# Kernel tuning notes

Measured on AMD Instinct MI355X. Metric: run time of the kernel, lower is better.

The kernel has to match this reference:

```python
import jax, jax.numpy as jnp
import numpy as np

EPS = 1e-6
THRESHOLD = 0.99
MAX_STEPS = 4
MIN_STEPS = 1
N_HEAD = 8
B, N, D, V, L, F, RCF = 1, 256, 512, 32000, 2, 1536, 2048


def rmsnorm(x, w):
    return x * jax.lax.rsqrt(jnp.mean(x * x, axis=-1, keepdims=True) + EPS) * w


def rope(x, base=10000.0):
    # x: [B, N, H, hd] -> rotary embedding (rotate-half convention)
    n, hd = x.shape[1], x.shape[-1]
    half = hd // 2
    inv = 1.0 / (base ** (jnp.arange(half, dtype=jnp.float32) * 2.0 / hd))
    ang = jnp.arange(n, dtype=jnp.float32)[:, None] * inv[None, :]  # [N, half]
    cos = jnp.cos(ang)[None, :, None, :]
    sin = jnp.sin(ang)[None, :, None, :]
    x1, x2 = x[..., :half], x[..., half:]
    return jnp.concatenate([x1 * cos - x2 * sin, x1 * sin + x2 * cos], axis=-1)


def attention(x, wqkv, wo):
    b, n, d = x.shape
    hd = d // N_HEAD
    q, k, v = jnp.split(x @ wqkv, 3, axis=-1)
    q = rope(q.reshape(b, n, N_HEAD, hd))
    k = rope(k.reshape(b, n, N_HEAD, hd))
    v = v.reshape(b, n, N_HEAD, hd)
    scores = jnp.einsum('bqhd,bkhd->bhqk', q, k) / np.float32(np.sqrt(hd))
    causal = jnp.tril(jnp.ones((n, n), dtype=bool))
    scores = jnp.where(causal, scores, jnp.float32(-1e30))
    a = jax.nn.softmax(scores, axis=-1)
    out = jnp.einsum('bhqk,bkhd->bqhd', a, v).reshape(b, n, d)
    return out @ wo


def backbone(input_ids, emb, attn_norm_w, mlp_norm_w, wqkv, wo, w_gate, w_up, w_down, final_norm_w):
    x = emb[input_ids]  # [B, N, D]
    for l in range(L):  # small fixed layer count
        x = x + attention(rmsnorm(x, attn_norm_w[l]), wqkv[l], wo[l])
        h = rmsnorm(x, mlp_norm_w[l])
        x = x + (jax.nn.silu(h @ w_gate[l]) * (h @ w_up[l])) @ w_down[l]  # SwiGLU
    return rmsnorm(x, final_norm_w)


def refinement_step(states, rc_norm_w, rc_w1, rc_w2, w_y, w_delta, w_halt, b_halt):
    h = rmsnorm(states, rc_norm_w)
    y_logits = h @ w_y                                   # [B, N, V]
    refined = states + jax.nn.gelu(h @ rc_w1) @ rc_w2    # [B, N, D]
    delta_logits = rmsnorm(refined, rc_norm_w) @ w_delta # [B, N, V]
    halt = jax.nn.sigmoid(h @ w_halt + b_halt)           # [B, N]
    combined = y_logits + delta_logits                   # compute_prediction
    return combined, halt, refined


def act_combine(halt_probs, step_logits):
    # Vectorized version of the per-(b,n) ACT halting loop.
    # halt_probs: [B, N, S]; step_logits: [B, N, S, V]
    p = halt_probs.at[..., :MIN_STEPS].set(0.0)  # min-step masking (max_steps > min_steps)
    cum = jnp.cumsum(p, axis=-1)
    prev = cum - p                      # exclusive cumulative halting prob
    running = prev < THRESHOLD          # step still executes
    is_last = jnp.arange(p.shape[-1]) == p.shape[-1] - 1
    use_rem = running & ((cum >= THRESHOLD) | is_last)  # halting step gets remainder
    weights = jnp.where(running, jnp.where(use_rem, 1.0 - prev, p), 0.0)
    final = jnp.einsum('bns,bnsv->bnv', weights, step_logits)
    remainder = jnp.sum(jnp.where(use_rem, 1.0 - prev, 0.0), axis=-1)
    ponder = jnp.sum(running, axis=-1).astype(p.dtype) + remainder  # N + R ponder cost
    return final, ponder, weights


def reference(input_ids, emb, attn_norm_w, mlp_norm_w, wqkv, wo, w_gate, w_up, w_down,
              final_norm_w, rc_norm_w, rc_w1, rc_w2, w_y, w_delta, w_halt, b_halt):
    hidden = backbone(input_ids, emb, attn_norm_w, mlp_norm_w, wqkv, wo,
                      w_gate, w_up, w_down, final_norm_w)
    states = hidden
    logits_steps, halt_steps = [], []
    for _ in range(MAX_STEPS):  # fixed refinement unroll
        combined, halt, states = refinement_step(states, rc_norm_w, rc_w1, rc_w2,
                                                 w_y, w_delta, w_halt, b_halt)
        logits_steps.append(combined)
        halt_steps.append(halt)
    step_logits = jnp.stack(logits_steps, axis=2)  # [B, N, S, V]
    halt_probs = jnp.stack(halt_steps, axis=2)     # [B, N, S]
    final_logits, ponder_costs, all_weights = act_combine(halt_probs, step_logits)
    return final_logits, ponder_costs, all_weights


def setup_inputs() -> dict:
    key = jax.random.key(0)
    ks = jax.random.split(key, 16)
    s = 0.02
    return {
        'input_ids': jax.random.randint(ks[0], (B, N), 0, V),
        'emb': jax.random.normal(ks[1], (V, D), jnp.float32) * s,
        'attn_norm_w': jnp.ones((L, D), jnp.float32),
        'mlp_norm_w': jnp.ones((L, D), jnp.float32),
        'wqkv': jax.random.normal(ks[2], (L, D, 3 * D), jnp.float32) * s,
        'wo': jax.random.normal(ks[3], (L, D, D), jnp.float32) * s,
        'w_gate': jax.random.normal(ks[4], (L, D, F), jnp.float32) * s,
        'w_up': jax.random.normal(ks[5], (L, D, F), jnp.float32) * s,
        'w_down': jax.random.normal(ks[6], (L, F, D), jnp.float32) * s,
        'final_norm_w': jnp.ones((D,), jnp.float32),
        'rc_norm_w': jnp.ones((D,), jnp.float32),
        'rc_w1': jax.random.normal(ks[7], (D, RCF), jnp.float32) * s,
        'rc_w2': jax.random.normal(ks[8], (RCF, D), jnp.float32) * s,
        'w_y': jax.random.normal(ks[9], (D, V), jnp.float32) * s,
        'w_delta': jax.random.normal(ks[10], (D, V), jnp.float32) * s,
        'w_halt': jax.random.normal(ks[11], (D,), jnp.float32) * s,
        'b_halt': jnp.zeros((), jnp.float32),
    }
```

## Files before the change

### kernel.cpp

```cpp
#include <hip/hip_runtime.h>
#include <hip/hip_bf16.h>

#define NTOK   256
#define DMODEL 512
#define NHEAD  8
#define HD     64
#define HALF   32
#define FF     1536
#define RCFF   2048
#define VOCAB  32000
#define NLAYER 2
#define NSTEPS 4
#define EPSV   1e-6f
#define THR    0.99f

typedef __attribute__((ext_vector_type(8))) short bf16x8;
typedef __attribute__((ext_vector_type(4))) float f32x4;

__global__ void k_embed(const int* __restrict__ ids, const float* __restrict__ emb,
                        float* __restrict__ x) {
    int row = blockIdx.x;
    int id = ids[row];
    for (int d = threadIdx.x; d < DMODEL; d += blockDim.x)
        x[row * DMODEL + d] = emb[(size_t)id * DMODEL + d];
}

__global__ __launch_bounds__(256) void k_rmsnorm(const float* __restrict__ in,
                                                 const float* __restrict__ w,
                                                 float* __restrict__ out) {
    int row = blockIdx.x;
    const float* xr = in + (size_t)row * DMODEL;
    float s = 0.f;
    for (int d = threadIdx.x; d < DMODEL; d += 256) { float v = xr[d]; s += v * v; }
    __shared__ float red[4];
    int lane = threadIdx.x & 63, wv = threadIdx.x >> 6;
    for (int o = 32; o > 0; o >>= 1) s += __shfl_xor(s, o);
    if (lane == 0) red[wv] = s;
    __syncthreads();
    float tot = red[0] + red[1] + red[2] + red[3];
    float scale = rsqrtf(tot * (1.f / DMODEL) + EPSV);
    for (int d = threadIdx.x; d < DMODEL; d += 256)
        out[(size_t)row * DMODEL + d] = xr[d] * scale * w[d];
}

__global__ __launch_bounds__(256) void k_mm_part(const float* __restrict__ A,
                                                 const float* __restrict__ W,
                                                 float* __restrict__ Cp,
                                                 int K, int N, int kc) {
    __shared__ float As[16][68];
    __shared__ float Ws[16][68];
    const int bn = blockIdx.x * 64;
    const int bm = blockIdx.y * 64;
    const int kz = blockIdx.z * kc;
    const int tx = threadIdx.x & 15;
    const int ty = threadIdx.x >> 4;
    float acc[4][4] = {};
    for (int k0 = kz; k0 < kz + kc; k0 += 16) {
#pragma unroll
        for (int r = 0; r < 4; ++r) {
            int idx = threadIdx.x + r * 256;
            int m = idx >> 4, kk = idx & 15;
            As[kk][m] = A[(size_t)(bm + m) * K + k0 + kk];
            int n = idx & 63, kw = idx >> 6;
            Ws[kw][n] = W[(size_t)(k0 + kw) * N + bn + n];
        }
        __syncthreads();
#pragma unroll
        for (int kk = 0; kk < 16; ++kk) {
            float4 av = *(const float4*)&As[kk][ty * 4];
            float4 bv = *(const float4*)&Ws[kk][tx * 4];
            float a[4] = {av.x, av.y, av.z, av.w};
            float b[4] = {bv.x, bv.y, bv.z, bv.w};
#pragma unroll
            for (int i = 0; i < 4; ++i)
#pragma unroll
                for (int j = 0; j < 4; ++j)
                    acc[i][j] = fmaf(a[i], b[j], acc[i][j]);
        }
        __syncthreads();
    }
    float* cp = Cp + (size_t)blockIdx.z * (size_t)(gridDim.y * 64) * N;
#pragma unroll
    for (int i = 0; i < 4; ++i) {
        int m = bm + ty * 4 + i;
#pragma unroll
        for (int j = 0; j < 4; ++j)
            cp[(size_t)m * N + bn + tx * 4 + j] = acc[i][j];
    }
}

__global__ __launch_bounds__(256) void k_gu_part(const float* __restrict__ A,
                                                 const float* __restrict__ Wg,
                                                 const float* __restrict__ Wu,
                                                 float* __restrict__ GU) {
    __shared__ float As[16][68];
    __shared__ float Ws[16][68];
    const int bn = blockIdx.x * 64;
    const int bm = blockIdx.y * 64;
    const int z = blockIdx.z;
    const float* W = (z >> 2) ? Wu : Wg;
    const int kz = (z & 3) * 128;
    const int tx = threadIdx.x & 15;
    const int ty = threadIdx.x >> 4;
    float acc[4][4] = {};
    for (int k0 = kz; k0 < kz + 128; k0 += 16) {
#pragma unroll
        for (int r = 0; r < 4; ++r) {
            int idx = threadIdx.x + r * 256;
            int m = idx >> 4, kk = idx & 15;
            As[kk][m] = A[(size_t)(bm + m) * DMODEL + k0 + kk];
            int n = idx & 63, kw = idx >> 6;
            Ws[kw][n] = W[(size_t)(k0 + kw) * FF + bn + n];
        }
        __syncthreads();
#pragma unroll
        for (int kk = 0; kk < 16; ++kk) {
            float4 av = *(const float4*)&As[kk][ty * 4];
            float4 bv = *(const float4*)&Ws[kk][tx * 4];
            float a[4] = {av.x, av.y, av.z, av.w};
            float b[4] = {bv.x, bv.y, bv.z, bv.w};
#pragma unroll
            for (int i = 0; i < 4; ++i)
#pragma unroll
                for (int j = 0; j < 4; ++j)
                    acc[i][j] = fmaf(a[i], b[j], acc[i][j]);
        }
        __syncthreads();
    }
    float* cp = GU + (size_t)z * (NTOK * FF);
#pragma unroll
    for (int i = 0; i < 4; ++i) {
        int m = bm + ty * 4 + i;
#pragma unroll
        for (int j = 0; j < 4; ++j)
            cp[(size_t)m * FF + bn + tx * 4 + j] = acc[i][j];
    }
}

__global__ void k_mm_finish(const float* __restrict__ Cp, const float* __restrict__ res,
                            float* __restrict__ C, int tot, int zstride, int nz, int act) {
    int i = blockIdx.x * 256 + threadIdx.x;
    if (i >= tot) return;
    float s = 0.f;
    for (int z = 0; z < nz; ++z) s += Cp[(size_t)z * zstride + i];
    if (res) s += res[i];
    if (act == 1) {
        float xg = s;
        float inner = 0.79788456080286536f * (xg + 0.044715f * xg * xg * xg);
        s = 0.5f * xg * (1.f + tanhf(inner));
    }
    C[i] = s;
}

__global__ void k_finish_silumul(const float* __restrict__ GU, float* __restrict__ C) {
    int i = blockIdx.x * 256 + threadIdx.x;
    float g = 0.f, u = 0.f;
#pragma unroll
    for (int z = 0; z < 4; ++z) {
        g += GU[(size_t)z * (NTOK * FF) + i];
        u += GU[(size_t)(z + 4) * (NTOK * FF) + i];
    }
    float sig = 1.f / (1.f + expf(-g));
    C[i] = g * sig * u;
}

__global__ __launch_bounds__(256) void k_finish_norm(const float* __restrict__ Cp,
                                                     const float* __restrict__ res,
                                                     const float* __restrict__ normw,
                                                     float* __restrict__ out_raw,
                                                     float* __restrict__ out_norm,
                                                     int nz) {
    int row = blockIdx.x, t = threadIdx.x;
    int c0 = t, c1 = t + 256;
    size_t base = (size_t)row * DMODEL;
    float v0 = 0.f, v1 = 0.f;
    for (int z = 0; z < nz; ++z) {
        size_t zb = (size_t)z * (NTOK * DMODEL) + base;
        v0 += Cp[zb + c0];
        v1 += Cp[zb + c1];
    }
    v0 += res[base + c0];
    v1 += res[base + c1];
    float ss = v0 * v0 + v1 * v1;
    __shared__ float red[4];
    int lane = t & 63, wv = t >> 6;
    for (int o = 32; o > 0; o >>= 1) ss += __shfl_xor(ss, o);
    if (lane == 0) red[wv] = ss;
    __syncthreads();
    float tot = red[0] + red[1] + red[2] + red[3];
    float scale = rsqrtf(tot * (1.f / DMODEL) + EPSV);
    out_raw[base + c0] = v0;
    out_raw[base + c1] = v1;
    out_norm[base + c0] = v0 * scale * normw[c0];
    out_norm[base + c1] = v1 * scale * normw[c1];
}

__global__ __launch_bounds__(256) void k_qkv_finish_rope(const float* __restrict__ Cp,
                                                         float* __restrict__ qkv) {
    int pos = blockIdx.x, t = threadIdx.x;
    int h = t >> 5, d = t & 31;
    size_t base = (size_t)pos * FF;
    auto S = [&](int col) {
        float s = 0.f;
#pragma unroll
        for (int z = 0; z < 4; ++z) s += Cp[(size_t)z * (NTOK * FF) + base + col];
        return s;
    };
    int cq0 = h * HD + d, cq1 = cq0 + HALF;
    int ck0 = DMODEL + cq0, ck1 = ck0 + HALF;
    int cv0 = 2 * DMODEL + t, cv1 = cv0 + 256;
    float q0 = S(cq0), q1 = S(cq1);
    float k0 = S(ck0), k1 = S(ck1);
    float v0 = S(cv0), v1 = S(cv1);
    float inv = powf(10000.f, -(float)d / 32.f);
    float ang = (float)pos * inv;
    float c = cosf(ang), s = sinf(ang);
    qkv[base + cq0] = q0 * c - q1 * s;
    qkv[base + cq1] = q0 * s + q1 * c;
    qkv[base + ck0] = k0 * c - k1 * s;
    qkv[base + ck1] = k0 * s + k1 * c;
    qkv[base + cv0] = v0;
    qkv[base + cv1] = v1;
}

__global__ __launch_bounds__(256) void k_attn(const float* __restrict__ qkv,
                                              float* __restrict__ out) {
    int h = blockIdx.x;
    int qi = blockIdx.y;
    int t = threadIdx.x;
    __shared__ float qs[HD];
    __shared__ float ps[NTOK];
    __shared__ float red[4];
    __shared__ float red2[4];
    __shared__ float os[4][HD];
    if (t < HD) qs[t] = qkv[(size_t)qi * FF + h * HD + t];
    __syncthreads();
    float sc = -1e30f;
    if (t <= qi) {
        const float* kr = qkv + (size_t)t * FF + DMODEL + h * HD;
        float s = 0.f;
        for (int d = 0; d < HD; ++d) s = fmaf(qs[d], kr[d], s);
        sc = s * 0.125f;
    }
    float m = sc;
    for (int o = 32; o > 0; o >>= 1) m = fmaxf(m, __shfl_xor(m, o));
    int lane = t & 63, wv = t >> 6;
    if (lane == 0) red[wv] = m;
    __syncthreads();
    m = fmaxf(fmaxf(red[0], red[1]), fmaxf(red[2], red[3]));
    float e = (t <= qi) ? expf(sc - m) : 0.f;
    ps[t] = e;
    float sum = e;
    for (int o = 32; o > 0; o >>= 1) sum += __shfl_xor(sum, o);
    if (lane == 0) red2[wv] = sum;
    __syncthreads();
    sum = red2[0] + red2[1] + red2[2] + red2[3];
    float inv = 1.f / sum;
    int d = t & 63, g = t >> 6;
    float acc = 0.f;
    for (int ki = g; ki <= qi; ki += 4)
        acc = fmaf(ps[ki], qkv[(size_t)ki * FF + 2 * DMODEL + h * HD + d], acc);
    os[g][d] = acc * inv;
    __syncthreads();
    if (t < HD)
        out[(size_t)qi * DMODEL + h * HD + t] = os[0][t] + os[1][t] + os[2][t] + os[3][t];
}

__global__ __launch_bounds__(256) void k_haltactab(const float* __restrict__ H,
                                                   const float* __restrict__ wh,
                                                   const float* __restrict__ bptr,
                                                   float* __restrict__ ponder_out,
                                                   float* __restrict__ w_out,
                                                   __hip_bfloat16* __restrict__ A,
                                                   __hip_bfloat16* __restrict__ Bm) {
    int i = blockIdx.x, t = threadIdx.x;
    int lane = t & 63, wv = t >> 6;
    __shared__ float red[4];
    __shared__ float hvals[3];
    __shared__ float hw[4];
    for (int s = 1; s <= 3; ++s) {
        const float* hr = H + ((size_t)s * NTOK + i) * DMODEL;
        float a = hr[t] * wh[t] + hr[t + 256] * wh[t + 256];
        for (int o = 32; o > 0; o >>= 1) a += __shfl_xor(a, o);
        if (lane == 0) red[wv] = a;
        __syncthreads();
        if (t == 0)
            hvals[s - 1] = 1.f / (1.f + expf(-(red[0] + red[1] + red[2] + red[3] + bptr[0])));
        __syncthreads();
    }
    if (t == 0) {
        float p[4] = {0.f, hvals[0], hvals[1], hvals[2]};
        float cum = 0.f, rem = 0.f;
        int nrun = 0;
#pragma unroll
        for (int s = 0; s < 4; ++s) {
            float prev = cum;
            cum += p[s];
            bool running = prev < THR;
            bool use_rem = running && ((cum >= THR) || (s == 3));
            float v = 0.f;
            if (running) {
                v = use_rem ? (1.f - prev) : p[s];
                if (use_rem) rem += (1.f - prev);
                nrun++;
            }
            hw[s] = v;
            w_out[i * 4 + s] = v;
        }
        ponder_out[i] = (float)nrun + rem;
    }
    __syncthreads();
    float w0 = hw[0], w1 = hw[1], w2 = hw[2], w3 = hw[3];
    size_t base = (size_t)i * DMODEL;
#pragma unroll
    for (int r = 0; r < 2; ++r) {
        int d = t + r * 256;
        float h0 = H[base + d];
        float h1 = H[(size_t)(NTOK * DMODEL) + base + d];
        float h2 = H[(size_t)(2 * NTOK * DMODEL) + base + d];
        float h3 = H[(size_t)(3 * NTOK * DMODEL) + base + d];
        float h4 = H[(size_t)(4 * NTOK * DMODEL) + base + d];
        A[base + d]  = __float2bfloat16(w0 * h0 + w1 * h1 + w2 * h2 + w3 * h3);
        Bm[base + d] = __float2bfloat16(w0 * h1 + w1 * h2 + w2 * h3 + w3 * h4);
    }
}

__global__ __launch_bounds__(512) void k_logits_mfma(const __hip_bfloat16* __restrict__ Abf,
                                                     const __hip_bfloat16* __restrict__ Bbf,
                                                     const float* __restrict__ Wy,
                                                     const float* __restrict__ Wd,
                                                     float* __restrict__ out) {
    __shared__ short Alds[256 * 32];
    __shared__ short Blds[256 * 32];
    __shared__ short Wys[32 * 70];
    __shared__ short Wds[32 * 70];
    const int tid  = threadIdx.x;
    const int wave = tid >> 6;
    const int lane = tid & 63;
    const int wrow = (wave & 1) * 128;
    const int wcol = (wave >> 1) * 16;
    const int cl   = lane & 15;
    const int kg   = lane >> 4;
    const int col  = blockIdx.x * 64 + wcol + cl;

    const int kr = tid >> 4;
    const int c4 = (tid & 15) * 4;
    const int sr0 = tid >> 2;
    const int skp = (tid & 3) * 8;

    f32x4 acc[8];
#pragma unroll
    for (int i = 0; i < 8; ++i) acc[i] = (f32x4){0.f, 0.f, 0.f, 0.f};

    const float* gy = Wy + (size_t)kr * VOCAB + blockIdx.x * 64 + c4;
    const float* gd = Wd + (size_t)kr * VOCAB + blockIdx.x * 64 + c4;

    float4 ry = *(const float4*)gy;
    float4 rd = *(const float4*)gd;
    bf16x8 ra0 = *(const bf16x8*)(Abf + (size_t)sr0 * DMODEL + skp);
    bf16x8 ra1 = *(const bf16x8*)(Abf + (size_t)(sr0 + 128) * DMODEL + skp);
    bf16x8 rb0 = *(const bf16x8*)(Bbf + (size_t)sr0 * DMODEL + skp);
    bf16x8 rb1 = *(const bf16x8*)(Bbf + (size_t)(sr0 + 128) * DMODEL + skp);

    for (int t = 0; t < 16; ++t) {
        __syncthreads();
        {
            short2 a, b;
            a.x = (short)__hip_bfloat16_raw(__float2bfloat16(ry.x)).x;
            a.y = (short)__hip_bfloat16_raw(__float2bfloat16(ry.y)).x;
            b.x = (short)__hip_bfloat16_raw(__float2bfloat16(ry.z)).x;
            b.y = (short)__hip_bfloat16_raw(__float2bfloat16(ry.w)).x;
            *(short2*)&Wys[kr * 70 + c4]     = a;
            *(short2*)&Wys[kr * 70 + c4 + 2] = b;
            a.x = (short)__hip_bfloat16_raw(__float2bfloat16(rd.x)).x;
            a.y = (short)__hip_bfloat16_raw(__float2bfloat16(rd.y)).x;
            b.x = (short)__hip_bfloat16_raw(__float2bfloat16(rd.z)).x;
            b.y = (short)__hip_bfloat16_raw(__float2bfloat16(rd.w)).x;
            *(short2*)&Wds[kr * 70 + c4]     = a;
            *(short2*)&Wds[kr * 70 + c4 + 2] = b;
            *(bf16x8*)&Alds[sr0 * 32 + skp]         = ra0;
            *(bf16x8*)&Alds[(sr0 + 128) * 32 + skp] = ra1;
            *(bf16x8*)&Blds[sr0 * 32 + skp]         = rb0;
            *(bf16x8*)&Blds[(sr0 + 128) * 32 + skp] = rb1;
        }
        if (t < 15) {
            const int kn = (t + 1) * 32;
            ry  = *(const float4*)(gy + (size_t)(t + 1) * 32 * VOCAB);
            rd  = *(const float4*)(gd + (size_t)(t + 1) * 32 * VOCAB);
            ra0 = *(const bf16x8*)(Abf + (size_t)sr0 * DMODEL + kn + skp);
            ra1 = *(const bf16x8*)(Abf + (size_t)(sr0 + 128) * DMODEL + kn + skp);
            rb0 = *(const bf16x8*)(Bbf + (size_t)sr0 * DMODEL + kn + skp);
            rb1 = *(const bf16x8*)(Bbf + (size_t)(sr0 + 128) * DMODEL + kn + skp);
        }
        __syncthreads();
        bf16x8 wy, wd;
#pragma unroll
        for (int j = 0; j < 8; ++j) {
            wy[j] = Wys[(kg * 8 + j) * 70 + wcol + cl];
            wd[j] = Wds[(kg * 8 + j) * 70 + wcol + cl];
        }
#pragma unroll
        for (int mt = 0; mt < 8; ++mt) {
            const int row = wrow + mt * 16 + cl;
            const bf16x8 a = *(const bf16x8*)&Alds[row * 32 + kg * 8];
            const bf16x8 b = *(const bf16x8*)&Blds[row * 32 + kg * 8];
            acc[mt] = __builtin_amdgcn_mfma_f32_16x16x32_bf16(a, wy, acc[mt], 0, 0, 0);
            acc[mt] = __builtin_amdgcn_mfma_f32_16x16x32_bf16(b, wd, acc[mt], 0, 0, 0);
        }
    }
#pragma unroll
    for (int mt = 0; mt < 8; ++mt)
#pragma unroll
        for (int r = 0; r < 4; ++r)
            out[(size_t)(wrow + mt * 16 + kg * 4 + r) * VOCAB + col] = acc[mt][r];
}

extern "C" void kernel_launch(void* const* d_in, const int* in_sizes, int n_in,
                              void* d_out, int out_size, void* d_ws, size_t ws_size,
                              hipStream_t stream) {
    const int*   ids          = (const int*)d_in[0];
    const float* emb          = (const float*)d_in[1];
    const float* attn_norm_w  = (const float*)d_in[2];
    const float* mlp_norm_w   = (const float*)d_in[3];
    const float* wqkv         = (const float*)d_in[4];
    const float* wo           = (const float*)d_in[5];
    const float* w_gate       = (const float*)d_in[6];
    const float* w_up         = (const float*)d_in[7];
    const float* w_down       = (const float*)d_in[8];
    const float* final_norm_w = (const float*)d_in[9];
    const float* rc_norm_w    = (const float*)d_in[10];
    const float* rc_w1        = (const float*)d_in[11];
    const float* rc_w2        = (const float*)d_in[12];
    const float* w_y          = (const float*)d_in[13];
    const float* w_delta      = (const float*)d_in[14];
    const float* w_halt       = (const float*)d_in[15];
    const float* b_halt       = (const float*)d_in[16];
    float* out = (float*)d_out;

    float* ws = (float*)d_ws;
    float* x       = ws + 0;
    float* xn      = ws + 131072;
    float* qkv     = ws + 262144;
    float* attnout = ws + 655360;
    float* g       = ws + 786432;
    float* t1      = ws + 1179648;
    float* states  = ws + 1703936;
    float* states2 = ws + 1835008;
    float* H       = ws + 1966080;
    __hip_bfloat16* Abf = (__hip_bfloat16*)(ws + 2623488);
    __hip_bfloat16* Bbf = (__hip_bfloat16*)(ws + 2754560);
    float* Cp      = ws + 2885632;
    float* GU      = ws + 1179648;

    k_embed<<<NTOK, 256, 0, stream>>>(ids, emb, x);
    k_rmsnorm<<<NTOK, 256, 0, stream>>>(x, attn_norm_w, xn);
    for (int l = 0; l < NLAYER; ++l) {
        k_mm_part<<<dim3(FF / 64, 4, 4), 256, 0, stream>>>(
            xn, wqkv + (size_t)l * DMODEL * FF, Cp, DMODEL, FF, 128);
        k_qkv_finish_rope<<<NTOK, 256, 0, stream>>>(Cp, qkv);
        k_attn<<<dim3(NHEAD, NTOK), 256, 0, stream>>>(qkv, attnout);
        k_mm_part<<<dim3(DMODEL / 64, 4, 8), 256, 0, stream>>>(
            attnout, wo + (size_t)l * DMODEL * DMODEL, Cp, DMODEL, DMODEL, 64);
        k_finish_norm<<<NTOK, 256, 0, stream>>>(Cp, x, mlp_norm_w + l * DMODEL, x, xn, 8);
        k_gu_part<<<dim3(FF / 64, 4, 8), 256, 0, stream>>>(
            xn, w_gate + (size_t)l * DMODEL * FF, w_up + (size_t)l * DMODEL * FF, GU);
        k_finish_silumul<<<NTOK * FF / 256, 256, 0, stream>>>(GU, g);
        k_mm_part<<<dim3(DMODEL / 64, 4, 12), 256, 0, stream>>>(
            g, w_down + (size_t)l * FF * DMODEL, Cp, FF, DMODEL, 128);
        const float* nw = (l == 0) ? (attn_norm_w + DMODEL) : final_norm_w;
        float* nout = (l == 0) ? xn : states;
        k_finish_norm<<<NTOK, 256, 0, stream>>>(Cp, x, nw, x, nout, 12);
    }

    k_rmsnorm<<<NTOK, 256, 0, stream>>>(states, rc_norm_w, H);
    float* scur = states;
    float* snxt = states2;
    for (int s = 0; s < NSTEPS; ++s) {
        k_mm_part<<<dim3(RCFF / 64, 4, 4), 256, 0, stream>>>(
            H + (size_t)s * NTOK * DMODEL, rc_w1, Cp, DMODEL, RCFF, 128);
        k_mm_finish<<<NTOK * RCFF / 256, 256, 0, stream>>>(
            Cp, nullptr, t1, NTOK * RCFF, NTOK * RCFF, 4, 1);
        k_mm_part<<<dim3(DMODEL / 64, 4, 16), 256, 0, stream>>>(
            t1, rc_w2, Cp, RCFF, DMODEL, 128);
        k_finish_norm<<<NTOK, 256, 0, stream>>>(
            Cp, scur, rc_norm_w, snxt, H + (size_t)(s + 1) * NTOK * DMODEL, 16);
        float* tmp = scur; scur = snxt; snxt = tmp;
    }

    k_haltactab<<<NTOK, 256, 0, stream>>>(H, w_halt, b_halt,
                                          out + (size_t)NTOK * VOCAB,
                                          out + (size_t)NTOK * VOCAB + NTOK,
                                          Abf, Bbf);

    k_logits_mfma<<<VOCAB / 64, 512, 0, stream>>>(Abf, Bbf, w_y, w_delta, out);
}
```

Baseline: 382.3 us.

## Enlarge fp32 GEMM M-tile to 128 with float4 loads; split logits over rows

The fp32 SIMT GEMM kernels now compute 128x64 tiles, eight rows per thread, and load A and W with float4 global reads. This is meant to raise arithmetic intensity and cut global load instructions, at the cost of more registers and half as many blocks. The MFMA logits kernel is split into two row halves on a 2D grid, doubling block count for occupancy but loading each W tile twice.

After: 475.2 us. +24.3%, slower.

```diff
diff --git a/kernel.cpp b/kernel.cpp
--- a/kernel.cpp
+++ b/kernel.cpp
@@ -43,84 +43,98 @@
         out[(size_t)row * DMODEL + d] = xr[d] * scale * w[d];
 }
 
-__global__ __launch_bounds__(256) void k_mm_part(const float* __restrict__ A,
-                                                 const float* __restrict__ W,
-                                                 float* __restrict__ Cp,
-                                                 int K, int N, int kc) {
-    __shared__ float As[16][68];
+__global__ __launch_bounds__(256) void k_mm_part2(const float* __restrict__ A,
+                                                  const float* __restrict__ W,
+                                                  float* __restrict__ Cp,
+                                                  int K, int N, int kc) {
+    __shared__ float As[16][132];
     __shared__ float Ws[16][68];
     const int bn = blockIdx.x * 64;
-    const int bm = blockIdx.y * 64;
+    const int bm = blockIdx.y * 128;
     const int kz = blockIdx.z * kc;
     const int tx = threadIdx.x & 15;
     const int ty = threadIdx.x >> 4;
-    float acc[4][4] = {};
+    float acc[8][4] = {};
     for (int k0 = kz; k0 < kz + kc; k0 += 16) {
 #pragma unroll
-        for (int r = 0; r < 4; ++r) {
-            int idx = threadIdx.x + r * 256;
-            int m = idx >> 4, kk = idx & 15;
-            As[kk][m] = A[(size_t)(bm + m) * K + k0 + kk];
-            int n = idx & 63, kw = idx >> 6;
-            Ws[kw][n] = W[(size_t)(k0 + kw) * N + bn + n];
+        for (int r = 0; r < 2; ++r) {
+            int f = threadIdx.x + r * 256;
+            int row = f >> 2, kq = (f & 3) * 4;
+            float4 v = *(const float4*)&A[(size_t)(bm + row) * K + k0 + kq];
+            As[kq + 0][row] = v.x;
+            As[kq + 1][row] = v.y;
+            As[kq + 2][row] = v.z;
+            As[kq + 3][row] = v.w;
+        }
+        {
+            int kw = threadIdx.x >> 4, n4 = (threadIdx.x & 15) * 4;
+            *(float4*)&Ws[kw][n4] = *(const float4*)&W[(size_t)(k0 + kw) * N + bn + n4];
         }
         __syncthreads();
 #pragma unroll
         for (int kk = 0; kk < 16; ++kk) {
-            float4 av = *(const float4*)&As[kk][ty * 4];
+            float4 a0 = *(const float4*)&As[kk][ty * 8];
+            float4 a1 = *(const float4*)&As[kk][ty * 8 + 4];
             float4 bv = *(const float4*)&Ws[kk][tx * 4];
-            float a[4] = {av.x, av.y, av.z, av.w};
+            float a[8] = {a0.x, a0.y, a0.z, a0.w, a1.x, a1.y, a1.z, a1.w};
             float b[4] = {bv.x, bv.y, bv.z, bv.w};
 #pragma unroll
-            for (int i = 0; i < 4; ++i)
+            for (int i = 0; i < 8; ++i)
 #pragma unroll
                 for (int j = 0; j < 4; ++j)
                     acc[i][j] = fmaf(a[i], b[j], acc[i][j]);
         }
         __syncthreads();
     }
-    float* cp = Cp + (size_t)blockIdx.z * (size_t)(gridDim.y * 64) * N;
-#pragma unroll
-    for (int i = 0; i < 4; ++i) {
-        int m = bm + ty * 4 + i;
+    float* cp = Cp + (size_t)blockIdx.z * (size_t)(gridDim.y * 128) * N;
+#pragma unroll
+    for (int i = 0; i < 8; ++i) {
+        int m = bm + ty * 8 + i;
 #pragma unroll
         for (int j = 0; j < 4; ++j)
             cp[(size_t)m * N + bn + tx * 4 + j] = acc[i][j];
     }
 }
 
-__global__ __launch_bounds__(256) void k_gu_part(const float* __restrict__ A,
-                                                 const float* __restrict__ Wg,
-                                                 const float* __restrict__ Wu,
-                                                 float* __restrict__ GU) {
-    __shared__ float As[16][68];
+__global__ __launch_bounds__(256) void k_gu_part2(const float* __restrict__ A,
+                                                  const float* __restrict__ Wg,
+                                                  const float* __restrict__ Wu,
+                                                  float* __restrict__ GU) {
+    __shared__ float As[16][132];
     __shared__ float Ws[16][68];
     const int bn = blockIdx.x * 64;
-    const int bm = blockIdx.y * 64;
+    const int bm = blockIdx.y * 128;
     const int z = blockIdx.z;
     const float* W = (z >> 2) ? Wu : Wg;
     const int kz = (z & 3) * 128;
     const int tx = threadIdx.x & 15;
     const int ty = threadIdx.x >> 4;
-    float acc[4][4] = {};
+    float acc[8][4] = {};
     for (int k0 = kz; k0 < kz + 128; k0 += 16) {
 #pragma unroll
-        for (int r = 0; r < 4; ++r) {
-            int idx = threadIdx.x + r * 256;
-            int m = idx >> 4, kk = idx & 15;
-            As[kk][m] = A[(size_t)(bm + m) * DMODEL + k0 + kk];
-            int n = idx & 63, kw = idx >> 6;
-            Ws[kw][n] = W[(size_t)(k0 + kw) * FF + bn + n];
+        for (int r = 0; r < 2; ++r) {
+            int f = threadIdx.x + r * 256;
+            int row = f >> 2, kq = (f & 3) * 4;
+            float4 v = *(const float4*)&A[(size_t)(bm + row) * DMODEL + k0 + kq];
+            As[kq + 0][row] = v.x;
+            As[kq + 1][row] = v.y;
+            As[kq + 2][row] = v.z;
+            As[kq + 3][row] = v.w;
+        }
+        {
+            int kw = threadIdx.x >> 4, n4 = (threadIdx.x & 15) * 4;
+            *(float4*)&Ws[kw][n4] = *(const float4*)&W[(size_t)(k0 + kw) * FF + bn + n4];
         }
         __syncthreads();
 #pragma unroll
         for (int kk = 0; kk < 16; ++kk) {
-            float4 av = *(const float4*)&As[kk][ty * 4];
+            float4 a0 = *(const float4*)&As[kk][ty * 8];
+            float4 a1 = *(const float4*)&As[kk][ty * 8 + 4];
             float4 bv = *(const float4*)&Ws[kk][tx * 4];
-            float a[4] = {av.x, av.y, av.z, av.w};
+            float a[8] = {a0.x, a0.y, a0.z, a0.w, a1.x, a1.y, a1.z, a1.w};
             float b[4] = {bv.x, bv.y, bv.z, bv.w};
 #pragma unroll
-            for (int i = 0; i < 4; ++i)
+            for (int i = 0; i < 8; ++i)
 #pragma unroll
                 for (int j = 0; j < 4; ++j)
                     acc[i][j] = fmaf(a[i], b[j], acc[i][j]);
@@ -129,8 +143,8 @@
     }
     float* cp = GU + (size_t)z * (NTOK * FF);
 #pragma unroll
-    for (int i = 0; i < 4; ++i) {
-        int m = bm + ty * 4 + i;
+    for (int i = 0; i < 8; ++i) {
+        int m = bm + ty * 8 + i;
 #pragma unroll
         for (int j = 0; j < 4; ++j)
             cp[(size_t)m * FF + bn + tx * 4 + j] = acc[i][j];
@@ -330,14 +344,15 @@
                                                      const float* __restrict__ Wy,
                                                      const float* __restrict__ Wd,
                                                      float* __restrict__ out) {
-    __shared__ short Alds[256 * 32];
-    __shared__ short Blds[256 * 32];
+    __shared__ short Alds[128 * 32];
+    __shared__ short Blds[128 * 32];
     __shared__ short Wys[32 * 70];
     __shared__ short Wds[32 * 70];
     const int tid  = threadIdx.x;
     const int wave = tid >> 6;
     const int lane = tid & 63;
-    const int wrow = (wave & 1) * 128;
+    const int rbase = blockIdx.y * 128;
+    const int wrow = (wave & 1) * 64;
     const int wcol = (wave >> 1) * 16;
     const int cl   = lane & 15;
     const int kg   = lane >> 4;
@@ -345,22 +360,20 @@
 
     const int kr = tid >> 4;
     const int c4 = (tid & 15) * 4;
-    const int sr0 = tid >> 2;
+    const int sr = tid >> 2;
     const int skp = (tid & 3) * 8;
 
-    f32x4 acc[8];
-#pragma unroll
-    for (int i = 0; i < 8; ++i) acc[i] = (f32x4){0.f, 0.f, 0.f, 0.f};
+    f32x4 acc[4];
+#pragma unroll
+    for (int i = 0; i < 4; ++i) acc[i] = (f32x4){0.f, 0.f, 0.f, 0.f};
 
     const float* gy = Wy + (size_t)kr * VOCAB + blockIdx.x * 64 + c4;
     const float* gd = Wd + (size_t)kr * VOCAB + blockIdx.x * 64 + c4;
 
     float4 ry = *(const float4*)gy;
     float4 rd = *(const float4*)gd;
-    bf16x8 ra0 = *(const bf16x8*)(Abf + (size_t)sr0 * DMODEL + skp);
-    bf16x8 ra1 = *(const bf16x8*)(Abf + (size_t)(sr0 + 128) * DMODEL + skp);
-    bf16x8 rb0 = *(const bf16x8*)(Bbf + (size_t)sr0 * DMODEL + skp);
-    bf16x8 rb1 = *(const bf16x8*)(Bbf + (size_t)(sr0 + 128) * DMODEL + skp);
+    bf16x8 ra = *(const bf16x8*)(Abf + (size_t)(rbase + sr) * DMODEL + skp);
+    bf16x8 rb = *(const bf16x8*)(Bbf + (size_t)(rbase + sr) * DMODEL + skp);
 
     for (int t = 0; t < 16; ++t) {
         __syncthreads();
@@ -378,19 +391,15 @@
             b.y = (short)__hip_bfloat16_raw(__float2bfloat16(rd.w)).x;
             *(short2*)&Wds[kr * 70 + c4]     = a;
             *(short2*)&Wds[kr * 70 + c4 + 2] = b;
-            *(bf16x8*)&Alds[sr0 * 32 + skp]         = ra0;
-            *(bf16x8*)&Alds[(sr0 + 128) * 32 + skp] = ra1;
-            *(bf16x8*)&Blds[sr0 * 32 + skp]         = rb0;
-            *(bf16x8*)&Blds[(sr0 + 128) * 32 + skp] = rb1;
+            *(bf16x8*)&Alds[sr * 32 + skp] = ra;
+            *(bf16x8*)&Blds[sr * 32 + skp] = rb;
         }
         if (t < 15) {
             const int kn = (t + 1) * 32;
-            ry  = *(const float4*)(gy + (size_t)(t + 1) * 32 * VOCAB);
-            rd  = *(const float4*)(gd + (size_t)(t + 1) * 32 * VOCAB);
-            ra0 = *(const bf16x8*)(Abf + (size_t)sr0 * DMODEL + kn + skp);
-            ra1 = *(const bf16x8*)(Abf + (size_t)(sr0 + 128) * DMODEL + kn + skp);
-            rb0 = *(const bf16x8*)(Bbf + (size_t)sr0 * DMODEL + kn + skp);
-            rb1 = *(const bf16x8*)(Bbf + (size_t)(sr0 + 128) * DMODEL + kn + skp);
+            ry = *(const float4*)(gy + (size_t)(t + 1) * 32 * VOCAB);
+            rd = *(const float4*)(gd + (size_t)(t + 1) * 32 * VOCAB);
+            ra = *(const bf16x8*)(Abf + (size_t)(rbase + sr) * DMODEL + kn + skp);
+            rb = *(const bf16x8*)(Bbf + (size_t)(rbase + sr) * DMODEL + kn + skp);
         }
         __syncthreads();
         bf16x8 wy, wd;
@@ -400,7 +409,7 @@
             wd[j] = Wds[(kg * 8 + j) * 70 + wcol + cl];
         }
 #pragma unroll
-        for (int mt = 0; mt < 8; ++mt) {
+        for (int mt = 0; mt < 4; ++mt) {
             const int row = wrow + mt * 16 + cl;
             const bf16x8 a = *(const bf16x8*)&Alds[row * 32 + kg * 8];
             const bf16x8 b = *(const bf16x8*)&Blds[row * 32 + kg * 8];
@@ -409,10 +418,10 @@
         }
     }
 #pragma unroll
-    for (int mt = 0; mt < 8; ++mt)
+    for (int mt = 0; mt < 4; ++mt)
 #pragma unroll
         for (int r = 0; r < 4; ++r)
-            out[(size_t)(wrow + mt * 16 + kg * 4 + r) * VOCAB + col] = acc[mt][r];
+            out[(size_t)(rbase + wrow + mt * 16 + kg * 4 + r) * VOCAB + col] = acc[mt][r];
 }
 
 extern "C" void kernel_launch(void* const* d_in, const int* in_sizes, int n_in,
@@ -455,17 +464,17 @@
     k_embed<<<NTOK, 256, 0, stream>>>(ids, emb, x);
     k_rmsnorm<<<NTOK, 256, 0, stream>>>(x, attn_norm_w, xn);
     for (int l = 0; l < NLAYER; ++l) {
-        k_mm_part<<<dim3(FF / 64, 4, 4), 256, 0, stream>>>(
+        k_mm_part2<<<dim3(FF / 64, 2, 4), 256, 0, stream>>>(
             xn, wqkv + (size_t)l * DMODEL * FF, Cp, DMODEL, FF, 128);
         k_qkv_finish_rope<<<NTOK, 256, 0, stream>>>(Cp, qkv);
         k_attn<<<dim3(NHEAD, NTOK), 256, 0, stream>>>(qkv, attnout);
-        k_mm_part<<<dim3(DMODEL / 64, 4, 8), 256, 0, stream>>>(
+        k_mm_part2<<<dim3(DMODEL / 64, 2, 8), 256, 0, stream>>>(
             attnout, wo + (size_t)l * DMODEL * DMODEL, Cp, DMODEL, DMODEL, 64);
         k_finish_norm<<<NTOK, 256, 0, stream>>>(Cp, x, mlp_norm_w + l * DMODEL, x, xn, 8);
-        k_gu_part<<<dim3(FF / 64, 4, 8), 256, 0, stream>>>(
+        k_gu_part2<<<dim3(FF / 64, 2, 8), 256, 0, stream>>>(
             xn, w_gate + (size_t)l * DMODEL * FF, w_up + (size_t)l * DMODEL * FF, GU);
         k_finish_silumul<<<NTOK * FF / 256, 256, 0, stream>>>(GU, g);
-        k_mm_part<<<dim3(DMODEL / 64, 4, 12), 256, 0, stream>>>(
+        k_mm_part2<<<dim3(DMODEL / 64, 2, 12), 256, 0, stream>>>(
             g, w_down + (size_t)l * FF * DMODEL, Cp, FF, DMODEL, 128);
         const float* nw = (l == 0) ? (attn_norm_w + DMODEL) : final_norm_w;
         float* nout = (l == 0) ? xn : states;
@@ -476,11 +485,11 @@
     float* scur = states;
     float* snxt = states2;
     for (int s = 0; s < NSTEPS; ++s) {
-        k_mm_part<<<dim3(RCFF / 64, 4, 4), 256, 0, stream>>>(
+        k_mm_part2<<<dim3(RCFF / 64, 2, 4), 256, 0, stream>>>(
             H + (size_t)s * NTOK * DMODEL, rc_w1, Cp, DMODEL, RCFF, 128);
         k_mm_finish<<<NTOK * RCFF / 256, 256, 0, stream>>>(
             Cp, nullptr, t1, NTOK * RCFF, NTOK * RCFF, 4, 1);
-        k_mm_part<<<dim3(DMODEL / 64, 4, 16), 256, 0, stream>>>(
+        k_mm_part2<<<dim3(DMODEL / 64, 2, 16), 256, 0, stream>>>(
             t1, rc_w2, Cp, RCFF, DMODEL, 128);
         k_finish_norm<<<NTOK, 256, 0, stream>>>(
             Cp, scur, rc_norm_w, snxt, H + (size_t)(s + 1) * NTOK * DMODEL, 16);
@@ -492,5 +501,5 @@
                                           out + (size_t)NTOK * VOCAB + NTOK,
                                           Abf, Bbf);
 
-    k_logits_mfma<<<VOCAB / 64, 512, 0, stream>>>(Abf, Bbf, w_y, w_delta, out);
-}
+    k_logits_mfma<<<dim3(VOCAB / 64, 2), 512, 0, stream>>>(Abf, Bbf, w_y, w_delta, out);
+}
```

## Fuse split-K reductions and activations into the next matmul's operand load

Applied to the files above, without the earlier changes.

Drops the standalone SiLU-mul and GELU finish kernels. The down-projection and rc_w2 matmuls now sum the split-K partials and apply the activation while loading their A tiles. This saves the intermediate global writes and reads and two launches, but the reduction and activation are recomputed by every column block. Split counts change for gate/up, down and rc_w2. Embedding and the first RMSNorm are merged into one kernel. The logits kernel stores W tiles transposed in LDS so fragments come from single vector reads, and its MFMA loop is unrolled by hand.

Result: slower. 733.9 us (+92.0%).

```diff
diff --git a/kernel.cpp b/kernel.cpp
--- a/kernel.cpp
+++ b/kernel.cpp
@@ -17,12 +17,32 @@
 typedef __attribute__((ext_vector_type(8))) short bf16x8;
 typedef __attribute__((ext_vector_type(4))) float f32x4;
 
-__global__ void k_embed(const int* __restrict__ ids, const float* __restrict__ emb,
-                        float* __restrict__ x) {
-    int row = blockIdx.x;
+__device__ __forceinline__ short f2b(float x) {
+    return (short)__hip_bfloat16_raw(__float2bfloat16(x)).x;
+}
+
+__global__ __launch_bounds__(256) void k_embed_norm(const int* __restrict__ ids,
+                                                    const float* __restrict__ emb,
+                                                    const float* __restrict__ w,
+                                                    float* __restrict__ x,
+                                                    float* __restrict__ xn) {
+    int row = blockIdx.x, t = threadIdx.x;
     int id = ids[row];
-    for (int d = threadIdx.x; d < DMODEL; d += blockDim.x)
-        x[row * DMODEL + d] = emb[(size_t)id * DMODEL + d];
+    const float* er = emb + (size_t)id * DMODEL;
+    float v0 = er[t], v1 = er[t + 256];
+    float ss = v0 * v0 + v1 * v1;
+    __shared__ float red[4];
+    int lane = t & 63, wv = t >> 6;
+    for (int o = 32; o > 0; o >>= 1) ss += __shfl_xor(ss, o);
+    if (lane == 0) red[wv] = ss;
+    __syncthreads();
+    float tot = red[0] + red[1] + red[2] + red[3];
+    float scale = rsqrtf(tot * (1.f / DMODEL) + EPSV);
+    size_t base = (size_t)row * DMODEL;
+    x[base + t] = v0;
+    x[base + t + 256] = v1;
+    xn[base + t] = v0 * scale * w[t];
+    xn[base + t + 256] = v1 * scale * w[t + 256];
 }
 
 __global__ __launch_bounds__(256) void k_rmsnorm(const float* __restrict__ in,
@@ -89,6 +109,66 @@
     }
 }
 
+__global__ __launch_bounds__(256) void k_mm_part_red(const float* __restrict__ Asrc,
+                                                     const float* __restrict__ W,
+                                                     float* __restrict__ Cp,
+                                                     int K, int N, int kc,
+                                                     int astride, int nred, int act) {
+    __shared__ float As[16][68];
+    __shared__ float Ws[16][68];
+    const int bn = blockIdx.x * 64;
+    const int bm = blockIdx.y * 64;
+    const int kz = blockIdx.z * kc;
+    const int tx = threadIdx.x & 15;
+    const int ty = threadIdx.x >> 4;
+    float acc[4][4] = {};
+    for (int k0 = kz; k0 < kz + kc; k0 += 16) {
+#pragma unroll
+        for (int r = 0; r < 4; ++r) {
+            int idx = threadIdx.x + r * 256;
+            int m = idx >> 4, kk = idx & 15;
+            size_t eoff = (size_t)(bm + m) * K + k0 + kk;
+            float v = 0.f;
+            for (int z = 0; z < nred; ++z) v += Asrc[(size_t)z * astride + eoff];
+            if (act == 1) {
+                float inner = 0.79788456080286536f * (v + 0.044715f * v * v * v);
+                v = 0.5f * v * (1.f + tanhf(inner));
+            } else {
+                float u = 0.f;
+                for (int z = 0; z < nred; ++z)
+                    u += Asrc[(size_t)(z + nred) * astride + eoff];
+                float sig = 1.f / (1.f + expf(-v));
+                v = v * sig * u;
+            }
+            As[kk][m] = v;
+            int n = idx & 63, kw = idx >> 6;
+            Ws[kw][n] = W[(size_t)(k0 + kw) * N + bn + n];
+        }
+        __syncthreads();
+#pragma unroll
+        for (int kk = 0; kk < 16; ++kk) {
+            float4 av = *(const float4*)&As[kk][ty * 4];
+            float4 bv = *(const float4*)&Ws[kk][tx * 4];
+            float a[4] = {av.x, av.y, av.z, av.w};
+            float b[4] = {bv.x, bv.y, bv.z, bv.w};
+#pragma unroll
+            for (int i = 0; i < 4; ++i)
+#pragma unroll
+                for (int j = 0; j < 4; ++j)
+                    acc[i][j] = fmaf(a[i], b[j], acc[i][j]);
+        }
+        __syncthreads();
+    }
+    float* cp = Cp + (size_t)blockIdx.z * (size_t)(gridDim.y * 64) * N;
+#pragma unroll
+    for (int i = 0; i < 4; ++i) {
+        int m = bm + ty * 4 + i;
+#pragma unroll
+        for (int j = 0; j < 4; ++j)
+            cp[(size_t)m * N + bn + tx * 4 + j] = acc[i][j];
+    }
+}
+
 __global__ __launch_bounds__(256) void k_gu_part(const float* __restrict__ A,
                                                  const float* __restrict__ Wg,
                                                  const float* __restrict__ Wu,
@@ -98,12 +178,12 @@
     const int bn = blockIdx.x * 64;
     const int bm = blockIdx.y * 64;
     const int z = blockIdx.z;
-    const float* W = (z >> 2) ? Wu : Wg;
-    const int kz = (z & 3) * 128;
+    const float* W = (z >> 1) ? Wu : Wg;
+    const int kz = (z & 1) * 256;
     const int tx = threadIdx.x & 15;
     const int ty = threadIdx.x >> 4;
     float acc[4][4] = {};
-    for (int k0 = kz; k0 < kz + 128; k0 += 16) {
+    for (int k0 = kz; k0 < kz + 256; k0 += 16) {
 #pragma unroll
         for (int r = 0; r < 4; ++r) {
             int idx = threadIdx.x + r * 256;
@@ -135,33 +215,6 @@
         for (int j = 0; j < 4; ++j)
             cp[(size_t)m * FF + bn + tx * 4 + j] = acc[i][j];
     }
-}
-
-__global__ void k_mm_finish(const float* __restrict__ Cp, const float* __restrict__ res,
-                            float* __restrict__ C, int tot, int zstride, int nz, int act) {
-    int i = blockIdx.x * 256 + threadIdx.x;
-    if (i >= tot) return;
-    float s = 0.f;
-    for (int z = 0; z < nz; ++z) s += Cp[(size_t)z * zstride + i];
-    if (res) s += res[i];
-    if (act == 1) {
-        float xg = s;
-        float inner = 0.79788456080286536f * (xg + 0.044715f * xg * xg * xg);
-        s = 0.5f * xg * (1.f + tanhf(inner));
-    }
-    C[i] = s;
-}
-
-__global__ void k_finish_silumul(const float* __restrict__ GU, float* __restrict__ C) {
-    int i = blockIdx.x * 256 + threadIdx.x;
-    float g = 0.f, u = 0.f;
-#pragma unroll
-    for (int z = 0; z < 4; ++z) {
-        g += GU[(size_t)z * (NTOK * FF) + i];
-        u += GU[(size_t)(z + 4) * (NTOK * FF) + i];
-    }
-    float sig = 1.f / (1.f + expf(-g));
-    C[i] = g * sig * u;
 }
 
 __global__ __launch_bounds__(256) void k_finish_norm(const float* __restrict__ Cp,
@@ -332,8 +385,8 @@
                                                      float* __restrict__ out) {
     __shared__ short Alds[256 * 32];
     __shared__ short Blds[256 * 32];
-    __shared__ short Wys[32 * 70];
-    __shared__ short Wds[32 * 70];
+    __shared__ short Wys[64 * 40];
+    __shared__ short Wds[64 * 40];
     const int tid  = threadIdx.x;
     const int wave = tid >> 6;
     const int lane = tid & 63;
@@ -365,19 +418,14 @@
     for (int t = 0; t < 16; ++t) {
         __syncthreads();
         {
-            short2 a, b;
-            a.x = (short)__hip_bfloat16_raw(__float2bfloat16(ry.x)).x;
-            a.y = (short)__hip_bfloat16_raw(__float2bfloat16(ry.y)).x;
-            b.x = (short)__hip_bfloat16_raw(__float2bfloat16(ry.z)).x;
-            b.y = (short)__hip_bfloat16_raw(__float2bfloat16(ry.w)).x;
-            *(short2*)&Wys[kr * 70 + c4]     = a;
-            *(short2*)&Wys[kr * 70 + c4 + 2] = b;
-            a.x = (short)__hip_bfloat16_raw(__float2bfloat16(rd.x)).x;
-            a.y = (short)__hip_bfloat16_raw(__float2bfloat16(rd.y)).x;
-            b.x = (short)__hip_bfloat16_raw(__float2bfloat16(rd.z)).x;
-            b.y = (short)__hip_bfloat16_raw(__float2bfloat16(rd.w)).x;
-            *(short2*)&Wds[kr * 70 + c4]     = a;
-            *(short2*)&Wds[kr * 70 + c4 + 2] = b;
+            Wys[(c4 + 0) * 40 + kr] = f2b(ry.x);
+            Wys[(c4 + 1) * 40 + kr] = f2b(ry.y);
+            Wys[(c4 + 2) * 40 + kr] = f2b(ry.z);
+            Wys[(c4 + 3) * 40 + kr] = f2b(ry.w);
+            Wds[(c4 + 0) * 40 + kr] = f2b(rd.x);
+            Wds[(c4 + 1) * 40 + kr] = f2b(rd.y);
+            Wds[(c4 + 2) * 40 + kr] = f2b(rd.z);
+            Wds[(c4 + 3) * 40 + kr] = f2b(rd.w);
             *(bf16x8*)&Alds[sr0 * 32 + skp]         = ra0;
             *(bf16x8*)&Alds[(sr0 + 128) * 32 + skp] = ra1;
             *(bf16x8*)&Blds[sr0 * 32 + skp]         = rb0;
@@ -393,19 +441,43 @@
             rb1 = *(const bf16x8*)(Bbf + (size_t)(sr0 + 128) * DMODEL + kn + skp);
         }
         __syncthreads();
-        bf16x8 wy, wd;
-#pragma unroll
-        for (int j = 0; j < 8; ++j) {
-            wy[j] = Wys[(kg * 8 + j) * 70 + wcol + cl];
-            wd[j] = Wds[(kg * 8 + j) * 70 + wcol + cl];
-        }
-#pragma unroll
-        for (int mt = 0; mt < 8; ++mt) {
-            const int row = wrow + mt * 16 + cl;
-            const bf16x8 a = *(const bf16x8*)&Alds[row * 32 + kg * 8];
-            const bf16x8 b = *(const bf16x8*)&Blds[row * 32 + kg * 8];
-            acc[mt] = __builtin_amdgcn_mfma_f32_16x16x32_bf16(a, wy, acc[mt], 0, 0, 0);
-            acc[mt] = __builtin_amdgcn_mfma_f32_16x16x32_bf16(b, wd, acc[mt], 0, 0, 0);
+        const bf16x8 wyf = *(const bf16x8*)&Wys[(wcol + cl) * 40 + kg * 8];
+        const bf16x8 wdf = *(const bf16x8*)&Wds[(wcol + cl) * 40 + kg * 8];
+        {
+            const bf16x8 a0 = *(const bf16x8*)&Alds[(wrow +  0 + cl) * 32 + kg * 8];
+            const bf16x8 a1 = *(const bf16x8*)&Alds[(wrow + 16 + cl) * 32 + kg * 8];
+            const bf16x8 a2 = *(const bf16x8*)&Alds[(wrow + 32 + cl) * 32 + kg * 8];
+            const bf16x8 a3 = *(const bf16x8*)&Alds[(wrow + 48 + cl) * 32 + kg * 8];
+            const bf16x8 b0 = *(const bf16x8*)&Blds[(wrow +  0 + cl) * 32 + kg * 8];
+            const bf16x8 b1 = *(const bf16x8*)&Blds[(wrow + 16 + cl) * 32 + kg * 8];
+            const bf16x8 b2 = *(const bf16x8*)&Blds[(wrow + 32 + cl) * 32 + kg * 8];
+            const bf16x8 b3 = *(const bf16x8*)&Blds[(wrow + 48 + cl) * 32 + kg * 8];
+            acc[0] = __builtin_amdgcn_mfma_f32_16x16x32_bf16(a0, wyf, acc[0], 0, 0, 0);
+            acc[0] = __builtin_amdgcn_mfma_f32_16x16x32_bf16(b0, wdf, acc[0], 0, 0, 0);
+            acc[1] = __builtin_amdgcn_mfma_f32_16x16x32_bf16(a1, wyf, acc[1], 0, 0, 0);
+            acc[1] = __builtin_amdgcn_mfma_f32_16x16x32_bf16(b1, wdf, acc[1], 0, 0, 0);
+            acc[2] = __builtin_amdgcn_mfma_f32_16x16x32_bf16(a2, wyf, acc[2], 0, 0, 0);
+            acc[2] = __builtin_amdgcn_mfma_f32_16x16x32_bf16(b2, wdf, acc[2], 0, 0, 0);
+            acc[3] = __builtin_amdgcn_mfma_f32_16x16x32_bf16(a3, wyf, acc[3], 0, 0, 0);
+            acc[3] = __builtin_amdgcn_mfma_f32_16x16x32_bf16(b3, wdf, acc[3], 0, 0, 0);
+        }
+        {
+            const bf16x8 a4 = *(const bf16x8*)&Alds[(wrow +  64 + cl) * 32 + kg * 8];
+            const bf16x8 a5 = *(const bf16x8*)&Alds[(wrow +  80 + cl) * 32 + kg * 8];
+            const bf16x8 a6 = *(const bf16x8*)&Alds[(wrow +  96 + cl) * 32 + kg * 8];
+            const bf16x8 a7 = *(const bf16x8*)&Alds[(wrow + 112 + cl) * 32 + kg * 8];
+            const bf16x8 b4 = *(const bf16x8*)&Blds[(wrow +  64 + cl) * 32 + kg * 8];
+            const bf16x8 b5 = *(const bf16x8*)&Blds[(wrow +  80 + cl) * 32 + kg * 8];
+            const bf16x8 b6 = *(const bf16x8*)&Blds[(wrow +  96 + cl) * 32 + kg * 8];
+            const bf16x8 b7 = *(const bf16x8*)&Blds[(wrow + 112 + cl) * 32 + kg * 8];
+            acc[4] = __builtin_amdgcn_mfma_f32_16x16x32_bf16(a4, wyf, acc[4], 0, 0, 0);
+            acc[4] = __builtin_amdgcn_mfma_f32_16x16x32_bf16(b4, wdf, acc[4], 0, 0, 0);
+            acc[5] = __builtin_amdgcn_mfma_f32_16x16x32_bf16(a5, wyf, acc[5], 0, 0, 0);
+            acc[5] = __builtin_amdgcn_mfma_f32_16x16x32_bf16(b5, wdf, acc[5], 0, 0, 0);
+            acc[6] = __builtin_amdgcn_mfma_f32_16x16x32_bf16(a6, wyf, acc[6], 0, 0, 0);
+            acc[6] = __builtin_amdgcn_mfma_f32_16x16x32_bf16(b6, wdf, acc[6], 0, 0, 0);
+            acc[7] = __builtin_amdgcn_mfma_f32_16x16x32_bf16(a7, wyf, acc[7], 0, 0, 0);
+            acc[7] = __builtin_amdgcn_mfma_f32_16x16x32_bf16(b7, wdf, acc[7], 0, 0, 0);
         }
     }
 #pragma unroll
@@ -442,8 +514,6 @@
     float* xn      = ws + 131072;
     float* qkv     = ws + 262144;
     float* attnout = ws + 655360;
-    float* g       = ws + 786432;
-    float* t1      = ws + 1179648;
     float* states  = ws + 1703936;
     float* states2 = ws + 1835008;
     float* H       = ws + 1966080;
@@ -451,9 +521,10 @@
     __hip_bfloat16* Bbf = (__hip_bfloat16*)(ws + 2754560);
     float* Cp      = ws + 2885632;
     float* GU      = ws + 1179648;
-
-    k_embed<<<NTOK, 256, 0, stream>>>(ids, emb, x);
-    k_rmsnorm<<<NTOK, 256, 0, stream>>>(x, attn_norm_w, xn);
+    float* CpD     = Cp;
+    float* Cp2     = ws + 0;
+
+    k_embed_norm<<<NTOK, 256, 0, stream>>>(ids, emb, attn_norm_w, x, xn);
     for (int l = 0; l < NLAYER; ++l) {
         k_mm_part<<<dim3(FF / 64, 4, 4), 256, 0, stream>>>(
             xn, wqkv + (size_t)l * DMODEL * FF, Cp, DMODEL, FF, 128);
@@ -462,14 +533,13 @@
         k_mm_part<<<dim3(DMODEL / 64, 4, 8), 256, 0, stream>>>(
             attnout, wo + (size_t)l * DMODEL * DMODEL, Cp, DMODEL, DMODEL, 64);
         k_finish_norm<<<NTOK, 256, 0, stream>>>(Cp, x, mlp_norm_w + l * DMODEL, x, xn, 8);
-        k_gu_part<<<dim3(FF / 64, 4, 8), 256, 0, stream>>>(
+        k_gu_part<<<dim3(FF / 64, 4, 4), 256, 0, stream>>>(
             xn, w_gate + (size_t)l * DMODEL * FF, w_up + (size_t)l * DMODEL * FF, GU);
-        k_finish_silumul<<<NTOK * FF / 256, 256, 0, stream>>>(GU, g);
-        k_mm_part<<<dim3(DMODEL / 64, 4, 12), 256, 0, stream>>>(
-            g, w_down + (size_t)l * FF * DMODEL, Cp, FF, DMODEL, 128);
+        k_mm_part_red<<<dim3(DMODEL / 64, 4, 8), 256, 0, stream>>>(
+            GU, w_down + (size_t)l * FF * DMODEL, CpD, FF, DMODEL, 192, NTOK * FF, 2, 2);
         const float* nw = (l == 0) ? (attn_norm_w + DMODEL) : final_norm_w;
         float* nout = (l == 0) ? xn : states;
-        k_finish_norm<<<NTOK, 256, 0, stream>>>(Cp, x, nw, x, nout, 12);
+        k_finish_norm<<<NTOK, 256, 0, stream>>>(CpD, x, nw, x, nout, 8);
     }
 
     k_rmsnorm<<<NTOK, 256, 0, stream>>>(states, rc_norm_w, H);
@@ -478,12 +548,10 @@
     for (int s = 0; s < NSTEPS; ++s) {
         k_mm_part<<<dim3(RCFF / 64, 4, 4), 256, 0, stream>>>(
             H + (size_t)s * NTOK * DMODEL, rc_w1, Cp, DMODEL, RCFF, 128);
-        k_mm_finish<<<NTOK * RCFF / 256, 256, 0, stream>>>(
-            Cp, nullptr, t1, NTOK * RCFF, NTOK * RCFF, 4, 1);
-        k_mm_part<<<dim3(DMODEL / 64, 4, 16), 256, 0, stream>>>(
-            t1, rc_w2, Cp, RCFF, DMODEL, 128);
+        k_mm_part_red<<<dim3(DMODEL / 64, 4, 8), 256, 0, stream>>>(
+            Cp, rc_w2, Cp2, RCFF, DMODEL, 256, NTOK * RCFF, 4, 1);
         k_finish_norm<<<NTOK, 256, 0, stream>>>(
-            Cp, scur, rc_norm_w, snxt, H + (size_t)(s + 1) * NTOK * DMODEL, 16);
+            Cp2, scur, rc_norm_w, snxt, H + (size_t)(s + 1) * NTOK * DMODEL, 8);
         float* tmp = scur; scur = snxt; snxt = tmp;
     }
 
```
